# Performance work log

Hardware: AMD Instinct MI355X
Metric: run time of the kernel (lower is better)

Reference implementation:

```python
import jax, jax.numpy as jnp
import numpy as np

N_NODES = 100000


def _gcn_conv(x, edge_index, W, b):
    # edge_index: [2, E] (src, dst). PyG GCNConv: add self-loops, symmetric norm.
    n = x.shape[0]
    src = jnp.concatenate([edge_index[0], jnp.arange(n, dtype=edge_index.dtype)])
    dst = jnp.concatenate([edge_index[1], jnp.arange(n, dtype=edge_index.dtype)])
    deg = jax.ops.segment_sum(jnp.ones_like(dst, dtype=x.dtype), dst, num_segments=n)
    dinv = jnp.where(deg > 0, jax.lax.rsqrt(deg), 0.0)
    norm = dinv[src] * dinv[dst]                      # [E+N]
    h = x @ W                                         # transform first (small dim)
    msg = h[src] * norm[:, None]                      # gather + normalize
    out = jax.ops.segment_sum(msg, dst, num_segments=n)  # scatter-aggregate
    return out + b


def setup_inputs() -> dict:
    key = jax.random.key(0)
    ks = jax.random.split(key, 8)
    x = jax.random.normal(ks[0], (N_NODES, 128), dtype=jnp.float32)
    edge_index = jax.random.randint(ks[1], (2, 1600000), 0, N_NODES, dtype=jnp.int32)
    def glorot(k, shape):
        lim = float(np.sqrt(6.0 / (shape[0] + shape[1])))
        return jax.random.uniform(k, shape, jnp.float32, -lim, lim)
    return {
        "x": x,
        "edge_index": edge_index,
        "W1": glorot(ks[2], (128, 64)),
        "b1": jnp.zeros((64,), jnp.float32),
        "W2": glorot(ks[3], (64, 64)),
        "b2": jnp.zeros((64,), jnp.float32),
        "Wh": glorot(ks[4], (64, 40)),
        "bh": jnp.zeros((40,), jnp.float32),
    }


def reference(x, edge_index, W1, b1, W2, b2, Wh, bh):
    # eval mode: dropout is identity
    h = jax.nn.relu(_gcn_conv(x, edge_index, W1, b1))
    h = jax.nn.relu(_gcn_conv(h, edge_index, W2, b2))
    return h @ Wh + bh  # [N, num_classes]
```

## Files before the change

### kernel.cpp

```cpp
#include <hip/hip_runtime.h>
#include <hip/hip_bf16.h>


#define BIN_SHIFT 9
#define BN        (1 << BIN_SHIFT)
#define NB_MAX    256
#define BIN_CHUNK 4096

typedef __attribute__((ext_vector_type(8))) short short8v;
typedef __attribute__((ext_vector_type(4))) float f32x4;

__device__ __forceinline__ float bf2f(unsigned short u) {
  union { unsigned i; float f; } c; c.i = ((unsigned)u) << 16; return c.f;
}
__device__ __forceinline__ unsigned short f2bf(float f) {
  union { float f; unsigned i; } c; c.f = f;
  unsigned r = c.i + 0x7FFFu + ((c.i >> 16) & 1u);
  return (unsigned short)(r >> 16);
}

__global__ __launch_bounds__(256) void k_zero(int* p, int n) {
  int i = blockIdx.x * blockDim.x + threadIdx.x;
  if (i < n) p[i] = 0;
}

__global__ __launch_bounds__(64) void k_zrow(unsigned short* hsS, int n) {
  int t = threadIdx.x;
  if (t < 64) {
    int s = t >> 4, f = t & 15;
    hsS[((size_t)s * (n + 1) + n) * 16 + f] = 0;
  }
}

__global__ __launch_bounds__(256) void k_bhist(const int* __restrict__ dst,
                                               int* bhist, int E, int nb) {
  __shared__ int lh[NB_MAX];
  lh[threadIdx.x] = 0;
  __syncthreads();
  for (int i = blockIdx.x * 256 + threadIdx.x; i < E; i += gridDim.x * 256)
    atomicAdd(&lh[dst[i] >> BIN_SHIFT], 1);
  __syncthreads();
  int v = lh[threadIdx.x];
  if (threadIdx.x < nb && v) atomicAdd(&bhist[threadIdx.x], v);
}

__global__ __launch_bounds__(256) void k_bscan(const int* __restrict__ bhist,
                                               int* boff, int* gcur, int nb, int E) {
  __shared__ int sh[256];
  const int t = threadIdx.x;
  int v = (t < nb) ? bhist[t] : 0;
  sh[t] = v;
  __syncthreads();
  for (int d = 1; d < 256; d <<= 1) {
    int x = (t >= d) ? sh[t - d] : 0;
    __syncthreads();
    sh[t] += x;
    __syncthreads();
  }
  if (t < nb) { int e = sh[t] - v; boff[t] = e; gcur[t] = e; }
  if (t == 0) boff[nb] = E;
}

__global__ __launch_bounds__(256) void k_bin(
    const int* __restrict__ src, const int* __restrict__ dst,
    int* gcur, int* __restrict__ binned, int E)
{
  __shared__ int  hist[NB_MAX];
  __shared__ int  excl[NB_MAX];
  __shared__ int  lcur[NB_MAX];
  __shared__ int  gbase[NB_MAX];
  __shared__ int2 stage[BIN_CHUNK];

  const int t = threadIdx.x;
  const int base = blockIdx.x * BIN_CHUNK;
  const int m = min(BIN_CHUNK, E - base);

  int2 pr[BIN_CHUNK / 256];
  int nmine = 0;
  #pragma unroll
  for (int i = 0; i < BIN_CHUNK / 256; ++i) {
    int idx = t + 256 * i;
    if (idx < m) {
      pr[i].x = src[base + idx];
      pr[i].y = dst[base + idx];
      nmine = i + 1;
    }
  }

  hist[t] = 0;
  __syncthreads();
  #pragma unroll
  for (int i = 0; i < BIN_CHUNK / 256; ++i)
    if (i < nmine) atomicAdd(&hist[pr[i].y >> BIN_SHIFT], 1);
  __syncthreads();

  const int mycnt = hist[t];
  for (int d = 1; d < 256; d <<= 1) {
    int v = (t >= d) ? hist[t - d] : 0;
    __syncthreads();
    hist[t] += v;
    __syncthreads();
  }
  {
    int e = hist[t] - mycnt;
    excl[t] = e;
    lcur[t] = e;
    gbase[t] = mycnt ? atomicAdd(&gcur[t], mycnt) : 0;
  }
  __syncthreads();

  #pragma unroll
  for (int i = 0; i < BIN_CHUNK / 256; ++i)
    if (i < nmine) {
      int b = pr[i].y >> BIN_SHIFT;
      int p = atomicAdd(&lcur[b], 1);
      stage[p] = pr[i];
    }
  __syncthreads();

  for (int i = t; i < m; i += 256) {
    int2 pp = stage[i];
    int b = pp.y >> BIN_SHIFT;
    binned[gbase[b] + (i - excl[b])] =
        (pp.x << BIN_SHIFT) | (pp.y & (BN - 1));
  }
}

__global__ __launch_bounds__(256) void k_csr(
    const int* __restrict__ binned, const int* __restrict__ boff,
    int* __restrict__ offs, int* __restrict__ endo,
    float* __restrict__ dinv, int* __restrict__ csr, int n)
{
  __shared__ int cnt_l[BN];
  __shared__ int tsum[256];
  __shared__ int lcur[BN];
  const int t = threadIdx.x;
  const int b = blockIdx.x;
  const int base = boff[b];
  const int end  = boff[b + 1];
  const int n0 = b << BIN_SHIFT;

  cnt_l[t] = 0; cnt_l[t + 256] = 0;
  __syncthreads();
  for (int i = base + t; i < end; i += 256)
    atomicAdd(&cnt_l[binned[i] & (BN - 1)], 1);
  __syncthreads();

  const int c0 = cnt_l[2 * t];
  const int c1 = cnt_l[2 * t + 1];
  const int s = c0 + c1;
  tsum[t] = s;
  __syncthreads();
  for (int d = 1; d < 256; d <<= 1) {
    int v = (t >= d) ? tsum[t - d] : 0;
    __syncthreads();
    tsum[t] += v;
    __syncthreads();
  }
  const int ex = tsum[t] - s;
  const int e0 = ex, e1 = ex + c0;
  const int g0 = n0 + 2 * t, g1 = g0 + 1;
  if (g0 < n) {
    offs[g0] = base + e0; endo[g0] = base + e1;
    dinv[g0] = rsqrtf((float)(c0 + 1));
  }
  if (g1 < n) {
    offs[g1] = base + e1; endo[g1] = base + e1 + c1;
    dinv[g1] = rsqrtf((float)(c1 + 1));
  }
  lcur[2 * t] = e0;
  lcur[2 * t + 1] = e1;
  __syncthreads();
  for (int i = base + t; i < end; i += 256) {
    int v = binned[i];
    int p = atomicAdd(&lcur[v & (BN - 1)], 1);
    csr[base + p] = v >> BIN_SHIFT;
  }
}

__global__ __launch_bounds__(256) void k_count(const int* __restrict__ dst, int* cnt, int E) {
  int e = blockIdx.x * blockDim.x + threadIdx.x;
  if (e < E) atomicAdd(&cnt[dst[e]], 1);
}
__global__ __launch_bounds__(256) void k_dinv(const int* __restrict__ cnt, float* dinv, int n) {
  int i = blockIdx.x * blockDim.x + threadIdx.x;
  if (i < n) dinv[i] = rsqrtf((float)(cnt[i] + 1));
}
__global__ __launch_bounds__(256) void k_scan1(const int* __restrict__ cnt,
                                               int* offs, int* bsum, int n) {
  __shared__ int sh[256];
  const int t = threadIdx.x;
  const int base = blockIdx.x * 1024 + t * 4;
  int v0 = 0, v1 = 0, v2 = 0, v3 = 0;
  if (base + 0 < n) v0 = cnt[base + 0];
  if (base + 1 < n) v1 = cnt[base + 1];
  if (base + 2 < n) v2 = cnt[base + 2];
  if (base + 3 < n) v3 = cnt[base + 3];
  const int s = v0 + v1 + v2 + v3;
  sh[t] = s;
  __syncthreads();
  for (int d = 1; d < 256; d <<= 1) {
    int x = (t >= d) ? sh[t - d] : 0;
    __syncthreads();
    sh[t] += x;
    __syncthreads();
  }
  int o = sh[t] - s;
  if (t == 255) bsum[blockIdx.x] = sh[255];
  if (base + 0 < n) { offs[base + 0] = o; o += v0; }
  if (base + 1 < n) { offs[base + 1] = o; o += v1; }
  if (base + 2 < n) { offs[base + 2] = o; o += v2; }
  if (base + 3 < n) { offs[base + 3] = o; o += v3; }
}
__global__ __launch_bounds__(256) void k_scan2(int* bsum, int nb) {
  __shared__ int sh[256];
  const int t = threadIdx.x;
  int v = (t < nb) ? bsum[t] : 0;
  sh[t] = v;
  __syncthreads();
  for (int d = 1; d < 256; d <<= 1) {
    int x = (t >= d) ? sh[t - d] : 0;
    __syncthreads();
    sh[t] += x;
    __syncthreads();
  }
  if (t < nb) bsum[t] = sh[t] - v;
}
__global__ __launch_bounds__(256) void k_scan3(int* offs, const int* __restrict__ bsum,
                                               int* cursor, int n) {
  int i = blockIdx.x * blockDim.x + threadIdx.x;
  if (i < n) {
    int o = offs[i] + bsum[i >> 10];
    offs[i] = o;
    cursor[i] = o;
  }
}
__global__ __launch_bounds__(256) void k_fill(const int* __restrict__ src,
                                              const int* __restrict__ dst,
                                              int* cursor, int* csr, int E) {
  int e = blockIdx.x * blockDim.x + threadIdx.x;
  if (e < E) {
    int p = atomicAdd(&cursor[dst[e]], 1);
    csr[p] = src[e];
  }
}

template<int K, int NOUT, bool SCALE, bool BIAS, bool OUTBF>
__global__ __launch_bounds__(256) void k_gemm(
    const float* __restrict__ X, const float* __restrict__ W,
    const float* __restrict__ dinv, const float* __restrict__ bias,
    void* __restrict__ Yv, int nrows, int nstride)
{
  constexpr int NCOL = (NOUT + 15) & ~15;
  constexpr int NT   = NCOL / 16;
  constexpr int KS   = K / 32;
  __shared__ __align__(16) unsigned short Xs[64 * K];
  __shared__ __align__(16) unsigned short WTs[NCOL * K];

  const int t = threadIdx.x;
  const int r0 = blockIdx.x * 64;

  if constexpr (NCOL != NOUT) {
    for (int i = t; i < (NCOL - NOUT) * K; i += 256)
      WTs[NOUT * K + i] = 0;
  }
  for (int idx = t; idx < K * NOUT; idx += 256) {
    int k = idx / NOUT, n = idx - k * NOUT;
    int u = (k >> 3) ^ (n & 7);
    WTs[n * K + u * 8 + (k & 7)] = f2bf(W[idx]);
  }
  for (int q = t; q < 16 * K; q += 256) {
    int row = q / (K / 4);
    int c4  = q - row * (K / 4);
    int gr  = r0 + row; if (gr >= nrows) gr = nrows - 1;
    float4 v = *(const float4*)&X[(size_t)gr * K + c4 * 4];
    int u = (c4 >> 1) ^ (row & 7);
    unsigned short* p = &Xs[row * K + u * 8 + (c4 & 1) * 4];
    p[0] = f2bf(v.x); p[1] = f2bf(v.y); p[2] = f2bf(v.z); p[3] = f2bf(v.w);
  }
  __syncthreads();

  const int wid  = t >> 6;
  const int lane = t & 63;
  const int l15  = lane & 15;
  const int kb   = lane >> 4;
  const int lrow = 16 * wid + l15;

  f32x4 acc[NT];
  #pragma unroll
  for (int j = 0; j < NT; ++j) { f32x4 z = {0.f, 0.f, 0.f, 0.f}; acc[j] = z; }

  #pragma unroll
  for (int ks = 0; ks < KS; ++ks) {
    const int ub = ks * 4 + kb;
    short8v a = *(const short8v*)&Xs[lrow * K + (ub ^ (lrow & 7)) * 8];
    #pragma unroll
    for (int j = 0; j < NT; ++j) {
      const int n = j * 16 + l15;
      short8v b = *(const short8v*)&WTs[n * K + (ub ^ (n & 7)) * 8];
      acc[j] = __builtin_amdgcn_mfma_f32_16x16x32_bf16(a, b, acc[j], 0, 0, 0);
    }
  }

  const int rbase = r0 + 16 * wid + kb * 4;
  #pragma unroll
  for (int r = 0; r < 4; ++r) {
    const int row = rbase + r;
    if (row >= nrows) continue;
    const float sc = SCALE ? dinv[row] : 1.f;
    #pragma unroll
    for (int j = 0; j < NT; ++j) {
      const int col = j * 16 + l15;
      if (col < NOUT) {
        float v = acc[j][r];
        if constexpr (SCALE) v *= sc;
        if constexpr (BIAS)  v += bias[col];
        if constexpr (OUTBF)
          ((unsigned short*)Yv)[((size_t)(col >> 4) * nstride + row) * 16 + (col & 15)] = f2bf(v);
        else
          ((float*)Yv)[(size_t)row * NOUT + col] = v;
      }
    }
  }
}

__global__ __launch_bounds__(256) void k_pull(
    const unsigned short* __restrict__ hsS, const int* __restrict__ csr,
    const int* __restrict__ offs, const int* __restrict__ endo,
    const float* __restrict__ dinv, const float* __restrict__ bias,
    float* __restrict__ out, int n)
{
  const int b     = blockIdx.x;
  const int slice = b & 3;
  const int wid   = threadIdx.x >> 6;
  const int lane  = threadIdx.x & 63;
  const int f     = lane & 15;
  const int node  = (b >> 2) * 16 + wid * 4 + (lane >> 4);
  const bool valid = node < n;
  const int nd    = valid ? node : 0;

  const unsigned short* hp = hsS + (size_t)slice * (n + 1) * 16;

  const int beg = offs[nd];
  const int m   = valid ? (endo[nd] - beg) : 0;

  int mmax = m;
  mmax = max(mmax, __shfl_xor(mmax, 16));
  mmax = max(mmax, __shfl_xor(mmax, 32));

  float acc = 0.f;
  for (int base = 0; base < mmax; base += 16) {
    int idx = (base + f < m) ? __builtin_nontemporal_load(&csr[beg + base + f]) : n;
    #pragma unroll
    for (int i = 0; i < 16; ++i) {
      int s = __shfl(idx, (lane & 48) + i);
      acc += bf2f(hp[(size_t)s * 16 + f]);
    }
  }

  if (valid) {
    acc += bf2f(hp[(size_t)nd * 16 + f]);
    float v = fmaf(dinv[nd], acc, bias[slice * 16 + f]);
    __builtin_nontemporal_store(fmaxf(v, 0.f),
                                &out[(size_t)nd * 64 + slice * 16 + f]);
  }
}

extern "C" void kernel_launch(void* const* d_in, const int* in_sizes, int n_in,
                              void* d_out, int out_size, void* d_ws, size_t ws_size,
                              hipStream_t stream) {
  const float* x  = (const float*)d_in[0];
  const int*   ei = (const int*)d_in[1];
  const float* W1 = (const float*)d_in[2];
  const float* b1 = (const float*)d_in[3];
  const float* W2 = (const float*)d_in[4];
  const float* b2 = (const float*)d_in[5];
  const float* Wh = (const float*)d_in[6];
  const float* bh = (const float*)d_in[7];
  float* out = (float*)d_out;

  const int N = in_sizes[0] / 128;
  const int E = in_sizes[1] / 2;
  const int* src = ei;
  const int* dst = ei + E;

  auto align_up = [](size_t v, size_t a) { return (v + a - 1) & ~(a - 1); };
  char* ws = (char*)d_ws;
  size_t off = 0;
  int*   cnt    = (int*)(ws + off);   off = align_up(off + (size_t)N * 4, 256);
  float* dinv   = (float*)(ws + off); off = align_up(off + (size_t)N * 4, 256);
  int*   offs   = (int*)(ws + off);   off = align_up(off + (size_t)N * 4, 256);
  int*   endo   = (int*)(ws + off);   off = align_up(off + (size_t)N * 4, 256);
  int*   bsum   = (int*)(ws + off);   off = align_up(off + 256 * 4, 256);
  int*   bhist  = (int*)(ws + off);   off = align_up(off + NB_MAX * 4, 256);
  int*   boff   = (int*)(ws + off);   off = align_up(off + (NB_MAX + 1) * 4, 256);
  int*   gcur   = (int*)(ws + off);   off = align_up(off + NB_MAX * 4, 256);
  int*   csr    = (int*)(ws + off);   off = align_up(off + (size_t)E * 4, 256);
  int*   binned = (int*)(ws + off);   off = align_up(off + (size_t)E * 4, 256);
  unsigned short* A = (unsigned short*)(ws + off);
  off = align_up(off + (size_t)(N + 1) * 64 * 2, 256);
  float* B      = (float*)(ws + off); off = align_up(off + (size_t)N * 64 * 4, 256);
  (void)ws_size;

  const int TB = 256;
  const int gN = (N + TB - 1) / TB;
  const int gE = (E + TB - 1) / TB;
  const int NBk = (N + BN - 1) >> BIN_SHIFT;
  const int gGemm = (N + 63) / 64;
  const int gPull = ((N + 15) / 16) * 4;
  const int gBin  = (E + BIN_CHUNK - 1) / BIN_CHUNK;
  const int NS = N + 1;

  k_zrow<<<1, 64, 0, stream>>>(A, N);

  if (NBk <= NB_MAX) {
    k_zero <<<1, TB, 0, stream>>>(bhist, NBk);
    k_bhist<<<512, TB, 0, stream>>>(dst, bhist, E, NBk);
    k_bscan<<<1, TB, 0, stream>>>(bhist, boff, gcur, NBk, E);
    k_bin  <<<gBin, TB, 0, stream>>>(src, dst, gcur, binned, E);
    k_csr  <<<NBk, TB, 0, stream>>>(binned, boff, offs, endo, dinv, csr, N);
  } else {
    k_zero <<<gN, TB, 0, stream>>>(cnt, N);
    k_count<<<gE, TB, 0, stream>>>(dst, cnt, E);
    k_dinv <<<gN, TB, 0, stream>>>(cnt, dinv, N);
    const int nb1 = (N + 1023) / 1024;
    k_scan1<<<nb1, TB, 0, stream>>>(cnt, offs, bsum, N);
    k_scan2<<<1,  TB, 0, stream>>>(bsum, nb1);
    k_scan3<<<gN, TB, 0, stream>>>(offs, bsum, endo, N);
    k_fill <<<gE, TB, 0, stream>>>(src, dst, endo, csr, E);
  }

  k_gemm<128, 64, true, false, true><<<gGemm, TB, 0, stream>>>(x, W1, dinv, nullptr, A, N, NS);
  k_pull<<<gPull, TB, 0, stream>>>(A, csr, offs, endo, dinv, b1, B, N);

  k_gemm<64, 64, true, false, true><<<gGemm, TB, 0, stream>>>(B, W2, dinv, nullptr, A, N, NS);
  k_pull<<<gPull, TB, 0, stream>>>(A, csr, offs, endo, dinv, b2, B, N);

  k_gemm<64, 40, false, true, false><<<gGemm, TB, 0, stream>>>(B, Wh, nullptr, bh, out, N, 0);
}
```

Measured before the change: 245.0 us.

## Restructure pull aggregation to one wave per node with vectorized edge-parallel gathers

Changes the CSR pull kernel from 16 lanes per node (one feature per lane, serial edges) to a full 64-lane wave per node, with 16 edges processed in parallel and each lane loading 4 bf16 features via an 8-byte load. Per-lane partial sums are combined with a cross-lane shuffle reduction, and the result is written as a float4. This targets the latency of serial dependent gathers and the use of narrow 2-byte loads, which matter with an average degree around 16. The cost is more blocks, the extra reduction, and mostly idle lanes on low-degree nodes.

```diff
diff --git a/kernel.cpp b/kernel.cpp
--- a/kernel.cpp
+++ b/kernel.cpp
@@ -334,35 +334,44 @@
   const int slice = b & 3;
   const int wid   = threadIdx.x >> 6;
   const int lane  = threadIdx.x & 63;
-  const int f     = lane & 15;
-  const int node  = (b >> 2) * 16 + wid * 4 + (lane >> 4);
-  const bool valid = node < n;
-  const int nd    = valid ? node : 0;
+  const int q     = lane & 3;
+  const int eg    = lane >> 2;
+  const int node  = (b >> 2) * 4 + wid;
+  if (node >= n) return;
 
   const unsigned short* hp = hsS + (size_t)slice * (n + 1) * 16;
 
-  const int beg = offs[nd];
-  const int m   = valid ? (endo[nd] - beg) : 0;
-
-  int mmax = m;
-  mmax = max(mmax, __shfl_xor(mmax, 16));
-  mmax = max(mmax, __shfl_xor(mmax, 32));
-
-  float acc = 0.f;
-  for (int base = 0; base < mmax; base += 16) {
-    int idx = (base + f < m) ? __builtin_nontemporal_load(&csr[beg + base + f]) : n;
-    #pragma unroll
-    for (int i = 0; i < 16; ++i) {
-      int s = __shfl(idx, (lane & 48) + i);
-      acc += bf2f(hp[(size_t)s * 16 + f]);
-    }
-  }
-
-  if (valid) {
-    acc += bf2f(hp[(size_t)nd * 16 + f]);
-    float v = fmaf(dinv[nd], acc, bias[slice * 16 + f]);
-    __builtin_nontemporal_store(fmaxf(v, 0.f),
-                                &out[(size_t)nd * 64 + slice * 16 + f]);
+  const int beg = offs[node];
+  const int m   = endo[node] - beg;
+
+  float a0 = 0.f, a1 = 0.f, a2 = 0.f, a3 = 0.f;
+
+  for (int base = 0; base < m; base += 16) {
+    const int e = base + eg;
+    const int s = (e < m) ? csr[beg + e] : n;
+    const uint2 u = *(const uint2*)&hp[(size_t)s * 16 + q * 4];
+    a0 += bf2f((unsigned short)u.x); a1 += bf2f((unsigned short)(u.x >> 16));
+    a2 += bf2f((unsigned short)u.y); a3 += bf2f((unsigned short)(u.y >> 16));
+  }
+
+  #pragma unroll
+  for (int d = 4; d <= 32; d <<= 1) {
+    a0 += __shfl_xor(a0, d); a1 += __shfl_xor(a1, d);
+    a2 += __shfl_xor(a2, d); a3 += __shfl_xor(a3, d);
+  }
+
+  if (lane < 4) {
+    const uint2 u = *(const uint2*)&hp[(size_t)node * 16 + q * 4];
+    a0 += bf2f((unsigned short)u.x); a1 += bf2f((unsigned short)(u.x >> 16));
+    a2 += bf2f((unsigned short)u.y); a3 += bf2f((unsigned short)(u.y >> 16));
+    const float dv = dinv[node];
+    const float4 bb = *(const float4*)&bias[slice * 16 + q * 4];
+    float4 o;
+    o.x = fmaxf(fmaf(dv, a0, bb.x), 0.f);
+    o.y = fmaxf(fmaf(dv, a1, bb.y), 0.f);
+    o.z = fmaxf(fmaf(dv, a2, bb.z), 0.f);
+    o.w = fmaxf(fmaf(dv, a3, bb.w), 0.f);
+    *(float4*)&out[(size_t)node * 64 + slice * 16 + q * 4] = o;
   }
 }
 
@@ -407,7 +416,7 @@
   const int gE = (E + TB - 1) / TB;
   const int NBk = (N + BN - 1) >> BIN_SHIFT;
   const int gGemm = (N + 63) / 64;
-  const int gPull = ((N + 15) / 16) * 4;
+  const int gPull = ((N + 3) / 4) * 4;
   const int gBin  = (E + BIN_CHUNK - 1) / BIN_CHUNK;
   const int NS = N + 1;
 
```

Result: slower. 339.5 us (+38.6%).
